# Optimization experiments

Measured on AMD Instinct MI355X. Metric: run time of the kernel, lower is better.

## Reference

```python
import jax, jax.numpy as jnp
import numpy as np

B, S, D = 4, 1024, 2048
N_HEADS, N_KV_HEADS = 32, 8
HEAD_DIM = D // N_HEADS          # 64
HALF = HEAD_DIM // 2             # 32
N_REP = N_HEADS // N_KV_HEADS    # 4


def setup_inputs() -> dict:
    key = jax.random.key(0)
    ks = jax.random.split(key, 6)
    # rotary tables: freqs_cis = exp(i * t * theta^( -2j/d )), real cos/sin halves
    inv_freq = 1.0 / (10000.0 ** (np.arange(0, HEAD_DIM, 2, dtype=np.float32) / HEAD_DIM))
    t = np.arange(S, dtype=np.float32)
    angles = np.outer(t, inv_freq)  # [S, HALF]
    return {
        "x": jax.random.normal(ks[0], (B, S, D), dtype=jnp.float32),
        "pos_cos": jnp.asarray(np.cos(angles), dtype=jnp.float32),
        "pos_sin": jnp.asarray(np.sin(angles), dtype=jnp.float32),
        "wq": jax.random.normal(ks[1], (D, N_HEADS * HEAD_DIM), dtype=jnp.float32) / np.sqrt(D),
        "wk": jax.random.normal(ks[2], (D, N_KV_HEADS * HEAD_DIM), dtype=jnp.float32) / np.sqrt(D),
        "wv": jax.random.normal(ks[3], (D, N_KV_HEADS * HEAD_DIM), dtype=jnp.float32) / np.sqrt(D),
        "wo": jax.random.normal(ks[4], (D, D), dtype=jnp.float32) / np.sqrt(D),
    }


def _apply_rotary(t, cos, sin):
    # t: [B, S, H, head_dim]; pairs of consecutive elements form complex numbers
    te = t[..., 0::2]  # real parts  [B,S,H,HALF]
    to = t[..., 1::2]  # imag parts
    c = cos[None, :, None, :]
    s = sin[None, :, None, :]
    re = te * c - to * s
    im = te * s + to * c
    return jnp.stack([re, im], axis=-1).reshape(t.shape)


def reference(x, pos_cos, pos_sin, wq, wk, wv, wo):
    b, s, d = x.shape
    xq = (x @ wq).reshape(b, s, N_HEADS, HEAD_DIM)
    xk = (x @ wk).reshape(b, s, N_KV_HEADS, HEAD_DIM)
    xv = (x @ wv).reshape(b, s, N_KV_HEADS, HEAD_DIM)
    xq = _apply_rotary(xq, pos_cos, pos_sin)
    xk = _apply_rotary(xk, pos_cos, pos_sin)
    # GQA: repeat kv heads (kv head h -> heads h*N_REP..h*N_REP+N_REP-1)
    xk = jnp.repeat(xk, N_REP, axis=2)
    xv = jnp.repeat(xv, N_REP, axis=2)
    scores = jnp.einsum("bqhd,bkhd->bhqk", xq, xk) / np.sqrt(HEAD_DIM).astype(np.float32)
    causal = jnp.triu(jnp.ones((s, s), dtype=bool), k=1)
    scores = jnp.where(causal[None, None], jnp.float32(-jnp.inf), scores)
    attn = jax.nn.softmax(scores.astype(jnp.float32), axis=-1).astype(x.dtype)
    out = jnp.einsum("bhqk,bkhd->bqhd", attn, xv).reshape(b, s, d)
    return out @ wo
```

## Files before the change

### kernel.cpp

```cpp
#include <hip/hip_runtime.h>
#include <hip/hip_bf16.h>


typedef __bf16 bf16x8 __attribute__((ext_vector_type(8)));
typedef float  f32x4  __attribute__((ext_vector_type(4)));
typedef unsigned short u16x8 __attribute__((ext_vector_type(8)));

#define DEV static __device__ __forceinline__

DEV unsigned short f2bf(float f) {
  __hip_bfloat16 h = __float2bfloat16(f);
  unsigned short u;
  __builtin_memcpy(&u, &h, 2);
  return u;
}
DEV float bf2f(unsigned short u) {
  unsigned int ui = ((unsigned int)u) << 16;
  float f;
  __builtin_memcpy(&f, &ui, 4);
  return f;
}

typedef const unsigned int __attribute__((address_space(1)))* as1_u32cp;
typedef unsigned int __attribute__((address_space(3)))* as3_u32p;

DEV void load16_lds(const unsigned short* g, unsigned short* l) {
  __builtin_amdgcn_global_load_lds((as1_u32cp)(unsigned long long)g,
                                   (as3_u32p)(unsigned int)(unsigned long long)l,
                                   16, 0, 0);
}

DEV f32x4 mfma16x16(bf16x8 a, bf16x8 b, f32x4 c) {
  return __builtin_amdgcn_mfma_f32_16x16x32_bf16(a, b, c, 0, 0, 0);
}

__global__ __launch_bounds__(256) void k_convert_x(const float* __restrict__ x,
                                                   unsigned short* __restrict__ xb, int n) {
  int i = (blockIdx.x * 256 + threadIdx.x) * 4;
  if (i < n) {
    float4 v = *(const float4*)(x + i);
    ushort4 o;
    o.x = f2bf(v.x); o.y = f2bf(v.y); o.z = f2bf(v.z); o.w = f2bf(v.w);
    *(ushort4*)(xb + i) = o;
  }
}

__global__ __launch_bounds__(256) void k_transpose_w(const float* __restrict__ src,
                                                     unsigned short* __restrict__ dst, int N) {
  __shared__ float t[32][33];
  const int n0 = blockIdx.x * 32, k0 = blockIdx.y * 32;
  const int tx = threadIdx.x & 31, ty = threadIdx.x >> 5;
#pragma unroll
  for (int i = 0; i < 4; i++) {
    int k = k0 + ty + i * 8;
    t[ty + i * 8][tx] = src[(size_t)k * N + n0 + tx];
  }
  __syncthreads();
#pragma unroll
  for (int i = 0; i < 4; i++) {
    int n = n0 + ty + i * 8;
    dst[(size_t)n * 2048 + k0 + tx] = f2bf(t[tx][ty + i * 8]);
  }
}

template <int OUTF32, int BN, int WM, int WN>
__global__ __launch_bounds__(512) void k_gemm8(const unsigned short* __restrict__ A,
                                               const unsigned short* __restrict__ Bt,
                                               void* __restrict__ Cp, int M, int N, int K) {
  constexpr int BM = 256;
  constexpr int FM = BM / WM / 16;
  constexpr int FN = BN / WN / 16;
  constexpr int LA = BM * 4 / 512;
  constexpr int LB = BN * 4 / 512;
  constexpr int LH = LA + LB;
  __shared__ __align__(16) unsigned short As[4][BM * 32];
  __shared__ __align__(16) unsigned short Bs[4][BN * 32];

  const int nbx = N / BN;
  const int nwg = gridDim.x;
  int wg = blockIdx.x;
  wg = (wg & 7) * (nwg >> 3) + (wg >> 3);
  const int bx = wg % nbx, by = wg / nbx;
  const int m0 = by << 8, n0 = bx * BN;
  const int tid = threadIdx.x;
  const int lane = tid & 63, wid = tid >> 6;
  const int wm = wid / WN, wn = wid % WN;
  const int l15 = lane & 15, kg = lane >> 4;
  const int H = K >> 5;
  const int NT = K >> 6;

  auto stageA = [&](int h, int i) {
    const int u = i * 512 + tid;
    const int row = u >> 2, sl = u & 3;
    const int gc = ((sl ^ ((row >> 1) & 3)) << 3);
    load16_lds(&A[(size_t)(m0 + row) * K + (h << 5) + gc],
               &As[h & 3][(i * 512 + (tid & ~63)) * 8]);
  };
  auto stageB = [&](int h, int i) {
    const int u = i * 512 + tid;
    const int row = u >> 2, sl = u & 3;
    const int gc = ((sl ^ ((row >> 1) & 3)) << 3);
    load16_lds(&Bt[(size_t)(n0 + row) * K + (h << 5) + gc],
               &Bs[h & 3][(i * 512 + (tid & ~63)) * 8]);
  };
  auto lda = [&](int s, int r) {
    return *(const bf16x8*)&As[s][r * 32 + ((kg ^ ((r >> 1) & 3)) << 3)];
  };
  auto ldb = [&](int s, int r) {
    return *(const bf16x8*)&Bs[s][r * 32 + ((kg ^ ((r >> 1) & 3)) << 3)];
  };

#define VMCNT_C2(c)                                                   \
  if ((c) == 2)      asm volatile("s_waitcnt vmcnt(%0)" ::"n"(2 * LH) : "memory"); \
  else if ((c) == 1) asm volatile("s_waitcnt vmcnt(%0)" ::"n"(LH) : "memory");     \
  else               asm volatile("s_waitcnt vmcnt(0)" ::: "memory");

  const int rowA0 = wm * (BM / WM) + l15;
  const int rowB0 = wn * (BN / WN) + l15;

  bf16x8 af[FM / 2], bf[FN];
  f32x4 acc[FM][FN] = {};

#pragma unroll
  for (int h = 0; h < 3; h++) {
    stageA(h, 0); stageA(h, 1);
    stageB(h, 0); if (LB > 1) stageB(h, 1);
  }
  asm volatile("s_waitcnt vmcnt(%0)" ::"n"(2 * LH) : "memory");
  __builtin_amdgcn_s_barrier();

  for (int t = 0; t < NT; t++) {
    const int s0 = (2 * t) & 3, s1 = (2 * t + 1) & 3;
    const int h3 = 2 * t + 3, h4 = 2 * t + 4;
    const bool v2 = (2 * t + 2) < H, v3 = h3 < H, v4 = h4 < H;

#pragma unroll
    for (int f = 0; f < FM / 2; f++) af[f] = lda(s0, rowA0 + f * 16);
#pragma unroll
    for (int g = 0; g < FN; g++) bf[g] = ldb(s0, rowB0 + g * 16);
    if (v3) { stageA(h3, 0); stageA(h3, 1); }
    __builtin_amdgcn_s_barrier();
    __builtin_amdgcn_s_setprio(1);
#pragma unroll
    for (int f = 0; f < FM / 2; f++)
#pragma unroll
      for (int g = 0; g < FN; g++) acc[f][g] = mfma16x16(af[f], bf[g], acc[f][g]);
    __builtin_amdgcn_s_setprio(0);

#pragma unroll
    for (int f = 0; f < FM / 2; f++) af[f] = lda(s0, rowA0 + (FM / 2 + f) * 16);
    if (v3) { stageB(h3, 0); if (LB > 1) stageB(h3, 1); }
    __builtin_amdgcn_s_barrier();
    __builtin_amdgcn_s_setprio(1);
#pragma unroll
    for (int f = 0; f < FM / 2; f++)
#pragma unroll
      for (int g = 0; g < FN; g++)
        acc[FM / 2 + f][g] = mfma16x16(af[f], bf[g], acc[FM / 2 + f][g]);
    __builtin_amdgcn_s_setprio(0);
    { const int c = (int)v2 + (int)v3; VMCNT_C2(c) }
    __builtin_amdgcn_s_barrier();

#pragma unroll
    for (int f = 0; f < FM / 2; f++) af[f] = lda(s1, rowA0 + f * 16);
#pragma unroll
    for (int g = 0; g < FN; g++) bf[g] = ldb(s1, rowB0 + g * 16);
    if (v4) { stageA(h4, 0); stageA(h4, 1); }
    __builtin_amdgcn_s_barrier();
    __builtin_amdgcn_s_setprio(1);
#pragma unroll
    for (int f = 0; f < FM / 2; f++)
#pragma unroll
      for (int g = 0; g < FN; g++) acc[f][g] = mfma16x16(af[f], bf[g], acc[f][g]);
    __builtin_amdgcn_s_setprio(0);

#pragma unroll
    for (int f = 0; f < FM / 2; f++) af[f] = lda(s1, rowA0 + (FM / 2 + f) * 16);
    if (v4) { stageB(h4, 0); if (LB > 1) stageB(h4, 1); }
    __builtin_amdgcn_s_barrier();
    __builtin_amdgcn_s_setprio(1);
#pragma unroll
    for (int f = 0; f < FM / 2; f++)
#pragma unroll
      for (int g = 0; g < FN; g++)
        acc[FM / 2 + f][g] = mfma16x16(af[f], bf[g], acc[FM / 2 + f][g]);
    __builtin_amdgcn_s_setprio(0);
    { const int c = (int)v3 + (int)v4; VMCNT_C2(c) }
    __builtin_amdgcn_s_barrier();
  }
#undef VMCNT_C2

  const int orow = m0 + wm * (BM / WM) + kg * 4;
#pragma unroll
  for (int fm = 0; fm < FM; fm++) {
#pragma unroll
    for (int fn = 0; fn < FN; fn++) {
      const int col = n0 + wn * (BN / WN) + fn * 16 + l15;
#pragma unroll
      for (int j = 0; j < 4; j++) {
        const size_t off = (size_t)(orow + fm * 16 + j) * N + col;
        if (OUTF32)
          ((float*)Cp)[off] = acc[fm][fn][j];
        else
          ((unsigned short*)Cp)[off] = f2bf(acc[fm][fn][j]);
      }
    }
  }
}

__global__ __launch_bounds__(256) void k_rope(unsigned short* __restrict__ qkv,
                                              const float* __restrict__ ctab,
                                              const float* __restrict__ stab) {
  const int idx = blockIdx.x * 256 + threadIdx.x;
  const int row = idx / 320;
  const int r = idx - row * 320;
  const int head = r >> 3, quad = r & 7;
  const int s = row & 1023;
  const int col = ((head < 32) ? head * 64 : 2048 + (head - 32) * 64) + quad * 8;
  const float4 c = *(const float4*)&ctab[s * 32 + quad * 4];
  const float4 sn = *(const float4*)&stab[s * 32 + quad * 4];
  const size_t base = (size_t)row * 3072 + col;
  u16x8 v = *(const u16x8*)&qkv[base];
  const float cc[4] = {c.x, c.y, c.z, c.w};
  const float ss[4] = {sn.x, sn.y, sn.z, sn.w};
#pragma unroll
  for (int i = 0; i < 4; i++) {
    const float e = bf2f(v[2 * i]), o = bf2f(v[2 * i + 1]);
    v[2 * i]     = f2bf(e * cc[i] - o * ss[i]);
    v[2 * i + 1] = f2bf(e * ss[i] + o * cc[i]);
  }
  *(u16x8*)&qkv[base] = v;
}

__global__ __launch_bounds__(256) void k_vt(const unsigned short* __restrict__ qkv,
                                            unsigned short* __restrict__ vt) {
  __shared__ unsigned short t[32][33];
  const int st0 = blockIdx.x * 32;
  const int d0 = blockIdx.y * 32;
  const int bkh = blockIdx.z;
  const int b = bkh >> 3, kh = bkh & 7;
  const int tx = threadIdx.x & 31, ty = threadIdx.x >> 5;
#pragma unroll
  for (int i = 0; i < 4; i++) {
    int s = st0 + ty + i * 8;
    t[ty + i * 8][tx] = qkv[(size_t)(b * 1024 + s) * 3072 + 2560 + kh * 64 + d0 + tx];
  }
  __syncthreads();
#pragma unroll
  for (int i = 0; i < 4; i++) {
    int d = d0 + ty + i * 8;
    vt[(size_t)(bkh * 64 + d) * 1024 + st0 + tx] = t[tx][ty + i * 8];
  }
}

__global__ __launch_bounds__(256) void k_attn(const unsigned short* __restrict__ qkv,
                                              const unsigned short* __restrict__ vt,
                                              unsigned short* __restrict__ ao) {
  __shared__ __align__(16) unsigned short Ks[2][64 * 64];
  __shared__ __align__(16) unsigned short Vs[2][64 * 64];
  __shared__ __align__(16) unsigned short P[4][16][64];

  const int bid = blockIdx.x;
  const int qt = 15 - (bid >> 7);
  const int hb = bid & 127;
  const int h = hb & 31, b = hb >> 5;
  const int q0 = qt << 6;
  const int wid = threadIdx.x >> 6, lane = threadIdx.x & 63;
  const int l15 = lane & 15, kg = lane >> 4;
  const int kh = h >> 2;
  const int qbase = b * 1024 + q0 + wid * 16;
  const int nt = qt + 1;
  const float NEGINF = -__builtin_inff();

  bf16x8 aq0, aq1;
  {
    const size_t qoff = (size_t)(qbase + l15) * 3072 + h * 64 + kg * 8;
    aq0 = *(const bf16x8*)&qkv[qoff];
    aq1 = *(const bf16x8*)&qkv[qoff + 32];
#pragma unroll
    for (int i = 0; i < 8; i++) {
      aq0[i] = (__bf16)((float)aq0[i] * 0.18033688011112042f);
      aq1[i] = (__bf16)((float)aq1[i] * 0.18033688011112042f);
    }
  }

  const int l8 = lane >> 3;
  const int colel = ((lane & 7) ^ l8) * 8;
  const size_t krowbase = (size_t)(b * 1024) * 3072 + 2048 + kh * 64 + colel;
  const size_t vrowbase = (size_t)((b * 8 + kh) * 64) * 1024 + colel;

#pragma unroll
  for (int i = 0; i < 2; i++) {
    const int r = wid * 16 + i * 8 + l8;
    load16_lds(&qkv[krowbase + (size_t)r * 3072], &Ks[0][(wid * 16 + i * 8) * 64]);
    load16_lds(&vt[vrowbase + (size_t)r * 1024], &Vs[0][(wid * 16 + i * 8) * 64]);
  }
  asm volatile("s_waitcnt vmcnt(0)" ::: "memory");
  __builtin_amdgcn_s_barrier();

  f32x4 o[4] = {};
  float mrow = NEGINF;
  float lrow = 0.f;

  const int swz = (l15 & 7) * 8;
  const int psw = (l15 & 7) * 8;

  for (int t = 0; t < nt; t++) {
    const int cur = t & 1;
    if (t + 1 < nt) {
      const size_t kv1 = (size_t)((t + 1) << 6);
#pragma unroll
      for (int i = 0; i < 2; i++) {
        const int r = wid * 16 + i * 8 + l8;
        load16_lds(&qkv[krowbase + (kv1 + r) * 3072], &Ks[cur ^ 1][(wid * 16 + i * 8) * 64]);
        load16_lds(&vt[vrowbase + (size_t)r * 1024 + kv1], &Vs[cur ^ 1][(wid * 16 + i * 8) * 64]);
      }
    }

    f32x4 sc[4] = {};
    __builtin_amdgcn_s_setprio(1);
#pragma unroll
    for (int ct = 0; ct < 4; ct++) {
      const unsigned short* kr = &Ks[cur][(ct * 16 + l15) * 64];
      bf16x8 bk0 = *(const bf16x8*)&kr[(kg * 8) ^ swz];
      bf16x8 bk1 = *(const bf16x8*)&kr[(kg * 8 + 32) ^ swz];
      sc[ct] = mfma16x16(bk0, aq0, sc[ct]);
      sc[ct] = mfma16x16(bk1, aq1, sc[ct]);
    }
    __builtin_amdgcn_s_setprio(0);

    float p[4][4];
    if (t == qt) {
      const int qloc = wid * 16 + l15;
#pragma unroll
      for (int ct = 0; ct < 4; ct++)
#pragma unroll
        for (int reg = 0; reg < 4; reg++) {
          const int kloc = ct * 16 + kg * 4 + reg;
          p[ct][reg] = (kloc > qloc) ? NEGINF : sc[ct][reg];
        }
    } else {
#pragma unroll
      for (int ct = 0; ct < 4; ct++)
#pragma unroll
        for (int reg = 0; reg < 4; reg++) p[ct][reg] = sc[ct][reg];
    }

    float rm = NEGINF;
#pragma unroll
    for (int ct = 0; ct < 4; ct++)
      rm = fmaxf(rm, fmaxf(fmaxf(p[ct][0], p[ct][1]), fmaxf(p[ct][2], p[ct][3])));
    rm = fmaxf(rm, __shfl_xor(rm, 16));
    rm = fmaxf(rm, __shfl_xor(rm, 32));

    const float mnew = fmaxf(mrow, rm);
    const float fac = exp2f(mrow - mnew);
    float rs = 0.f;
#pragma unroll
    for (int ct = 0; ct < 4; ct++)
#pragma unroll
      for (int reg = 0; reg < 4; reg++) {
        const float e = exp2f(p[ct][reg] - mnew);
        p[ct][reg] = e;
        rs += e;
      }
    rs += __shfl_xor(rs, 16);
    rs += __shfl_xor(rs, 32);
    lrow = lrow * fac + rs;
    mrow = mnew;
#pragma unroll
    for (int ct = 0; ct < 4; ct++) {
      o[ct][0] *= fac; o[ct][1] *= fac; o[ct][2] *= fac; o[ct][3] *= fac;
    }

#pragma unroll
    for (int ct = 0; ct < 4; ct++) {
      ushort4 pk;
      pk.x = f2bf(p[ct][0]); pk.y = f2bf(p[ct][1]);
      pk.z = f2bf(p[ct][2]); pk.w = f2bf(p[ct][3]);
      *(ushort4*)&P[wid][l15][(ct * 16 + kg * 4) ^ psw] = pk;
    }

    bf16x8 ap0 = *(const bf16x8*)&P[wid][l15][(kg * 8) ^ psw];
    bf16x8 ap1 = *(const bf16x8*)&P[wid][l15][(32 + kg * 8) ^ psw];

    __builtin_amdgcn_s_setprio(1);
#pragma unroll
    for (int ct = 0; ct < 4; ct++) {
      const unsigned short* vr = &Vs[cur][(ct * 16 + l15) * 64];
      bf16x8 bv0 = *(const bf16x8*)&vr[(kg * 8) ^ swz];
      bf16x8 bv1 = *(const bf16x8*)&vr[(kg * 8 + 32) ^ swz];
      o[ct] = mfma16x16(bv0, ap0, o[ct]);
      o[ct] = mfma16x16(bv1, ap1, o[ct]);
    }
    __builtin_amdgcn_s_setprio(0);

    asm volatile("s_waitcnt vmcnt(0)" ::: "memory");
    __builtin_amdgcn_s_barrier();
  }

  const float rl = 1.0f / lrow;
  const size_t obase = (size_t)(qbase + l15) * 2048 + h * 64;
#pragma unroll
  for (int ct = 0; ct < 4; ct++) {
    ushort4 ov;
    ov.x = f2bf(o[ct][0] * rl); ov.y = f2bf(o[ct][1] * rl);
    ov.z = f2bf(o[ct][2] * rl); ov.w = f2bf(o[ct][3] * rl);
    *(ushort4*)&ao[obase + ct * 16 + kg * 4] = ov;
  }
}

extern "C" void kernel_launch(void* const* d_in, const int* in_sizes, int n_in,
                              void* d_out, int out_size, void* d_ws, size_t ws_size,
                              hipStream_t stream) {
  const float* x    = (const float*)d_in[0];
  const float* pcos = (const float*)d_in[1];
  const float* psin = (const float*)d_in[2];
  const float* wq   = (const float*)d_in[3];
  const float* wk   = (const float*)d_in[4];
  const float* wv   = (const float*)d_in[5];
  const float* wo   = (const float*)d_in[6];

  char* ws = (char*)d_ws;
  unsigned short* XB  = (unsigned short*)(ws);
  unsigned short* WT  = (unsigned short*)(ws + 16777216);
  unsigned short* WOT = (unsigned short*)(ws + 29360128);
  unsigned short* QKV = (unsigned short*)(ws + 37748736);
  unsigned short* VT  = (unsigned short*)(ws + 62914560);

  k_convert_x<<<8192, 256, 0, stream>>>(x, XB, 8388608);
  k_transpose_w<<<dim3(64, 64), 256, 0, stream>>>(wq, WT, 2048);
  k_transpose_w<<<dim3(16, 64), 256, 0, stream>>>(wk, WT + (size_t)2048 * 2048, 512);
  k_transpose_w<<<dim3(16, 64), 256, 0, stream>>>(wv, WT + (size_t)2560 * 2048, 512);
  k_transpose_w<<<dim3(64, 64), 256, 0, stream>>>(wo, WOT, 2048);

  k_gemm8<0, 256, 2, 4><<<192, 512, 0, stream>>>(XB, WT, QKV, 4096, 3072, 2048);
  k_rope<<<5120, 256, 0, stream>>>(QKV, pcos, psin);
  k_vt<<<dim3(32, 2, 32), 256, 0, stream>>>(QKV, VT);
  k_attn<<<2048, 256, 0, stream>>>(QKV, VT, XB);
  k_gemm8<1, 128, 4, 2><<<256, 512, 0, stream>>>(XB, WOT, d_out, 4096, 2048, 2048);
}
```

Measured before the change: 277.9 us.

## Fuse RoPE and V-transpose into QKV GEMM epilogue, merge weight transposes

The QKV projection GEMM epilogue now applies rotary embedding to Q/K columns using a lane shuffle to fetch the paired element, and writes V columns directly in transposed layout into the VT buffer. This removes the separate k_rope and k_vt kernels and their extra global read/write passes over QKV. The three Q/K/V weight transposes are merged into one launch. In exchange, the epilogue does per-element cos/sin table loads and scattered 8-byte stores for V.

```diff
diff --git a/kernel.cpp b/kernel.cpp
--- a/kernel.cpp
+++ b/kernel.cpp
@@ -45,6 +45,31 @@
   }
 }
 
+__global__ __launch_bounds__(256) void k_transpose_qkv(const float* __restrict__ wq,
+                                                       const float* __restrict__ wk,
+                                                       const float* __restrict__ wv,
+                                                       unsigned short* __restrict__ dst) {
+  __shared__ float t[32][33];
+  const int n0 = blockIdx.x * 32, k0 = blockIdx.y * 32;
+  const float* src;
+  int nb, sN;
+  if (n0 < 2048)      { src = wq; nb = n0;        sN = 2048; }
+  else if (n0 < 2560) { src = wk; nb = n0 - 2048; sN = 512; }
+  else                { src = wv; nb = n0 - 2560; sN = 512; }
+  const int tx = threadIdx.x & 31, ty = threadIdx.x >> 5;
+#pragma unroll
+  for (int i = 0; i < 4; i++) {
+    int k = k0 + ty + i * 8;
+    t[ty + i * 8][tx] = src[(size_t)k * sN + nb + tx];
+  }
+  __syncthreads();
+#pragma unroll
+  for (int i = 0; i < 4; i++) {
+    int n = n0 + ty + i * 8;
+    dst[(size_t)n * 2048 + k0 + tx] = f2bf(t[tx][ty + i * 8]);
+  }
+}
+
 __global__ __launch_bounds__(256) void k_transpose_w(const float* __restrict__ src,
                                                      unsigned short* __restrict__ dst, int N) {
   __shared__ float t[32][33];
@@ -63,10 +88,14 @@
   }
 }
 
-template <int OUTF32, int BN, int WM, int WN>
+template <int MODE, int BN, int WM, int WN>
 __global__ __launch_bounds__(512) void k_gemm8(const unsigned short* __restrict__ A,
                                                const unsigned short* __restrict__ Bt,
-                                               void* __restrict__ Cp, int M, int N, int K) {
+                                               void* __restrict__ Cp,
+                                               unsigned short* __restrict__ vtp,
+                                               const float* __restrict__ ctab,
+                                               const float* __restrict__ stab,
+                                               int M, int N, int K) {
   constexpr int BM = 256;
   constexpr int FM = BM / WM / 16;
   constexpr int FN = BN / WN / 16;
@@ -191,65 +220,51 @@
 #undef VMCNT_C2
 
   const int orow = m0 + wm * (BM / WM) + kg * 4;
-#pragma unroll
-  for (int fm = 0; fm < FM; fm++) {
-#pragma unroll
-    for (int fn = 0; fn < FN; fn++) {
-      const int col = n0 + wn * (BN / WN) + fn * 16 + l15;
-#pragma unroll
-      for (int j = 0; j < 4; j++) {
-        const size_t off = (size_t)(orow + fm * 16 + j) * N + col;
-        if (OUTF32)
-          ((float*)Cp)[off] = acc[fm][fn][j];
-        else
-          ((unsigned short*)Cp)[off] = f2bf(acc[fm][fn][j]);
+  if (MODE == 1) {
+#pragma unroll
+    for (int fm = 0; fm < FM; fm++) {
+#pragma unroll
+      for (int fn = 0; fn < FN; fn++) {
+        const int col = n0 + wn * (BN / WN) + fn * 16 + l15;
+#pragma unroll
+        for (int j = 0; j < 4; j++)
+          ((float*)Cp)[(size_t)(orow + fm * 16 + j) * N + col] = acc[fm][fn][j];
       }
     }
-  }
-}
-
-__global__ __launch_bounds__(256) void k_rope(unsigned short* __restrict__ qkv,
-                                              const float* __restrict__ ctab,
-                                              const float* __restrict__ stab) {
-  const int idx = blockIdx.x * 256 + threadIdx.x;
-  const int row = idx / 320;
-  const int r = idx - row * 320;
-  const int head = r >> 3, quad = r & 7;
-  const int s = row & 1023;
-  const int col = ((head < 32) ? head * 64 : 2048 + (head - 32) * 64) + quad * 8;
-  const float4 c = *(const float4*)&ctab[s * 32 + quad * 4];
-  const float4 sn = *(const float4*)&stab[s * 32 + quad * 4];
-  const size_t base = (size_t)row * 3072 + col;
-  u16x8 v = *(const u16x8*)&qkv[base];
-  const float cc[4] = {c.x, c.y, c.z, c.w};
-  const float ss[4] = {sn.x, sn.y, sn.z, sn.w};
-#pragma unroll
-  for (int i = 0; i < 4; i++) {
-    const float e = bf2f(v[2 * i]), o = bf2f(v[2 * i + 1]);
-    v[2 * i]     = f2bf(e * cc[i] - o * ss[i]);
-    v[2 * i + 1] = f2bf(e * ss[i] + o * cc[i]);
-  }
-  *(u16x8*)&qkv[base] = v;
-}
-
-__global__ __launch_bounds__(256) void k_vt(const unsigned short* __restrict__ qkv,
-                                            unsigned short* __restrict__ vt) {
-  __shared__ unsigned short t[32][33];
-  const int st0 = blockIdx.x * 32;
-  const int d0 = blockIdx.y * 32;
-  const int bkh = blockIdx.z;
-  const int b = bkh >> 3, kh = bkh & 7;
-  const int tx = threadIdx.x & 31, ty = threadIdx.x >> 5;
-#pragma unroll
-  for (int i = 0; i < 4; i++) {
-    int s = st0 + ty + i * 8;
-    t[ty + i * 8][tx] = qkv[(size_t)(b * 1024 + s) * 3072 + 2560 + kh * 64 + d0 + tx];
-  }
-  __syncthreads();
-#pragma unroll
-  for (int i = 0; i < 4; i++) {
-    int d = d0 + ty + i * 8;
-    vt[(size_t)(bkh * 64 + d) * 1024 + st0 + tx] = t[tx][ty + i * 8];
+  } else if (MODE == 2 && n0 >= 2560) {
+#pragma unroll
+    for (int fm = 0; fm < FM; fm++) {
+      const int row0 = orow + fm * 16;
+      const int b = row0 >> 10, s0 = row0 & 1023;
+#pragma unroll
+      for (int fn = 0; fn < FN; fn++) {
+        const int vcol = n0 + wn * (BN / WN) + fn * 16 + l15 - 2560;
+        ushort4 ov;
+        ov.x = f2bf(acc[fm][fn][0]); ov.y = f2bf(acc[fm][fn][1]);
+        ov.z = f2bf(acc[fm][fn][2]); ov.w = f2bf(acc[fm][fn][3]);
+        *(ushort4*)&vtp[((size_t)((b * 8 + (vcol >> 6)) * 64 + (vcol & 63))) * 1024 + s0] = ov;
+      }
+    }
+  } else if (MODE == 2) {
+    unsigned short* Cq = (unsigned short*)Cp;
+#pragma unroll
+    for (int fm = 0; fm < FM; fm++) {
+#pragma unroll
+      for (int fn = 0; fn < FN; fn++) {
+        const int col = n0 + wn * (BN / WN) + fn * 16 + l15;
+        const int pair = (col & 63) >> 1;
+#pragma unroll
+        for (int j = 0; j < 4; j++) {
+          const int row = orow + fm * 16 + j;
+          const int s = row & 1023;
+          const float v = acc[fm][fn][j];
+          const float pv = __shfl_xor(v, 1);
+          const float c = ctab[s * 32 + pair], sn = stab[s * 32 + pair];
+          const float outv = (col & 1) ? (pv * sn + v * c) : (v * c - pv * sn);
+          Cq[(size_t)row * (size_t)N + col] = f2bf(outv);
+        }
+      }
+    }
   }
 }
 
@@ -429,14 +444,12 @@
   unsigned short* VT  = (unsigned short*)(ws + 62914560);
 
   k_convert_x<<<8192, 256, 0, stream>>>(x, XB, 8388608);
-  k_transpose_w<<<dim3(64, 64), 256, 0, stream>>>(wq, WT, 2048);
-  k_transpose_w<<<dim3(16, 64), 256, 0, stream>>>(wk, WT + (size_t)2048 * 2048, 512);
-  k_transpose_w<<<dim3(16, 64), 256, 0, stream>>>(wv, WT + (size_t)2560 * 2048, 512);
+  k_transpose_qkv<<<dim3(96, 64), 256, 0, stream>>>(wq, wk, wv, WT);
   k_transpose_w<<<dim3(64, 64), 256, 0, stream>>>(wo, WOT, 2048);
 
-  k_gemm8<0, 256, 2, 4><<<192, 512, 0, stream>>>(XB, WT, QKV, 4096, 3072, 2048);
-  k_rope<<<5120, 256, 0, stream>>>(QKV, pcos, psin);
-  k_vt<<<dim3(32, 2, 32), 256, 0, stream>>>(QKV, VT);
+  k_gemm8<2, 256, 2, 4><<<192, 512, 0, stream>>>(XB, WT, QKV, VT, pcos, psin,
+                                                 4096, 3072, 2048);
   k_attn<<<2048, 256, 0, stream>>>(QKV, VT, XB);
-  k_gemm8<1, 128, 4, 2><<<256, 512, 0, stream>>>(XB, WOT, d_out, 4096, 2048, 2048);
-}
+  k_gemm8<1, 128, 4, 2><<<256, 512, 0, stream>>>(XB, WOT, d_out, nullptr, nullptr, nullptr,
+                                                 4096, 2048, 2048);
+}
```

Result: faster. 271.5 us (-2.3%).
